# Optimization experiments

Measured on AMD Instinct MI355X. Metric: run time of the kernel, lower is better.

Reference implementation:

```python
import jax, jax.numpy as jnp
import numpy as np

N = 65536    # nodes per node type
E = 1048576  # edges per edge type
D = 512      # feature dim
B = 64       # graphs in batch


def _ln(x, g, b):
    m = x.mean(-1, keepdims=True)
    v = ((x - m) ** 2).mean(-1, keepdims=True)
    return (x - m) / jnp.sqrt(v + 1e-5) * g + b


def _seg_softmax(logits, seg, n):
    m = jax.ops.segment_max(logits, seg, num_segments=n)
    e = jnp.exp(logits - m[seg])
    s = jax.ops.segment_sum(e, seg, num_segments=n)
    return e / s[seg]


def setup_inputs():
    key = jax.random.key(0)
    k = jax.random.split(key, 16)
    sc = 1.0 / np.sqrt(D)
    d = {}
    d["x_inst"] = jax.random.normal(k[0], (N, D), jnp.float32)
    d["x_net"] = jax.random.normal(k[1], (N, D), jnp.float32)
    d["ln_g_inst"] = jnp.ones((D,), jnp.float32)
    d["ln_b_inst"] = jnp.zeros((D,), jnp.float32)
    d["ln_g_net"] = jnp.ones((D,), jnp.float32)
    d["ln_b_net"] = jnp.zeros((D,), jnp.float32)
    d["Wkqv_inst"] = jax.random.normal(k[2], (D, 3), jnp.float32) * sc
    d["bkqv_inst"] = jnp.zeros((3,), jnp.float32)
    d["Wkqv_net"] = jax.random.normal(k[3], (D, 3), jnp.float32) * sc
    d["bkqv_net"] = jnp.zeros((3,), jnp.float32)
    d["k_rel_w"] = jax.random.normal(k[4], (2,), jnp.float32)
    d["k_rel_b"] = jnp.zeros((2,), jnp.float32)
    d["v_rel_w"] = jax.random.normal(k[5], (2,), jnp.float32)
    d["v_rel_b"] = jnp.zeros((2,), jnp.float32)
    d["p_rel"] = jnp.ones((2,), jnp.float32)  # per-edge-type attention prior (heads=1)
    d["w_out_inst"] = jax.random.normal(k[6], (), jnp.float32)
    d["b_out_inst"] = jnp.zeros((), jnp.float32)
    d["w_out_net"] = jax.random.normal(k[7], (), jnp.float32)
    d["b_out_net"] = jnp.zeros((), jnp.float32)
    d["W_mlp_inst"] = jax.random.normal(k[8], (2 * D, D), jnp.float32) / np.sqrt(2 * D)
    d["b_mlp_inst"] = jnp.zeros((D,), jnp.float32)
    d["W_mlp_net"] = jax.random.normal(k[9], (2 * D, D), jnp.float32) / np.sqrt(2 * D)
    d["b_mlp_net"] = jnp.zeros((D,), jnp.float32)
    d["ei_i2n"] = jax.random.randint(k[10], (2, E), 0, N)
    d["ei_n2i"] = jax.random.randint(k[11], (2, E), 0, N)
    d["batch_inst"] = jnp.sort(jax.random.randint(k[12], (N,), 0, B))
    d["batch_net"] = jnp.sort(jax.random.randint(k[13], (N,), 0, B))
    return d


def _forward(x_inst, x_net, ln_g_inst, ln_b_inst, ln_g_net, ln_b_net,
             Wkqv_inst, bkqv_inst, Wkqv_net, bkqv_net,
             k_rel_w, k_rel_b, v_rel_w, v_rel_b, p_rel,
             w_out_inst, b_out_inst, w_out_net, b_out_net,
             W_mlp_inst, b_mlp_inst, W_mlp_net, b_mlp_net,
             ei_i2n, ei_n2i, batch_inst, batch_net):
    # LayerNorm per node over features
    xn_i = _ln(x_inst, ln_g_inst, ln_b_inst)
    xn_n = _ln(x_net, ln_g_net, ln_b_net)

    # HGTConv with out_channels=1, heads=1, head_dim=1: kqv are scalar per node
    kqv_i = xn_i @ Wkqv_inst + bkqv_inst  # [N, 3]
    kqv_n = xn_n @ Wkqv_net + bkqv_net
    k_i, q_i, v_i = kqv_i[:, 0], kqv_i[:, 1], kqv_i[:, 2]
    k_n, q_n, v_n = kqv_n[:, 0], kqv_n[:, 1], kqv_n[:, 2]

    def het_attn(k_src, v_src, q_dst, ei, rel):
        src, dst = ei[0], ei[1]
        kt = k_src * k_rel_w[rel] + k_rel_b[rel]  # per-relation K transform
        vt = v_src * v_rel_w[rel] + v_rel_b[rel]  # per-relation V transform
        # head_dim = 1 -> sqrt(D_head) = 1
        logits = q_dst[dst] * kt[src] * p_rel[rel]
        a = _seg_softmax(logits, dst, N)  # segment softmax over incoming edges
        return jax.ops.segment_sum(a * vt[src], dst, num_segments=N)  # [N]

    aggr_net = het_attn(k_i, v_i, q_n, ei_i2n, 0)   # edge type 0: inst -> net
    aggr_inst = het_attn(k_n, v_n, q_i, ei_n2i, 1)  # edge type 1: net -> inst

    # out_lin (1->1) + GELU; skip connection is skipped since 1 != D
    score_inst = jax.nn.gelu(aggr_inst * w_out_inst + b_out_inst, approximate=False)
    score_net = jax.nn.gelu(aggr_net * w_out_net + b_out_net, approximate=False)

    def pool(xn, score, batch, W, b):
        s = _seg_softmax(score, batch, B)              # softmax of scores per graph
        xw = xn * s[:, None]                           # [N, D]
        x_add = jax.ops.segment_sum(xw, batch, num_segments=B)
        x_max = jax.ops.segment_max(xw, batch, num_segments=B)
        return jnp.concatenate([x_add, x_max], axis=-1) @ W + b  # [B, D]

    out_inst = pool(xn_i, score_inst, batch_inst, W_mlp_inst, b_mlp_inst)
    out_net = pool(xn_n, score_net, batch_net, W_mlp_net, b_mlp_net)
    return jnp.concatenate([out_inst, out_net], axis=-1)  # [B, 2*D]


def reference(x_inst, x_net, ln_g_inst, ln_b_inst, ln_g_net, ln_b_net,
              Wkqv_inst, bkqv_inst, Wkqv_net, bkqv_net,
              k_rel_w, k_rel_b, v_rel_w, v_rel_b, p_rel,
              w_out_inst, b_out_inst, w_out_net, b_out_net,
              W_mlp_inst, b_mlp_inst, W_mlp_net, b_mlp_net,
              ei_i2n, ei_n2i, batch_inst, batch_net):
    return _forward(x_inst, x_net, ln_g_inst, ln_b_inst, ln_g_net, ln_b_net,
                    Wkqv_inst, bkqv_inst, Wkqv_net, bkqv_net,
                    k_rel_w, k_rel_b, v_rel_w, v_rel_b, p_rel,
                    w_out_inst, b_out_inst, w_out_net, b_out_net,
                    W_mlp_inst, b_mlp_inst, W_mlp_net, b_mlp_net,
                    ei_i2n, ei_n2i, batch_inst, batch_net)
```

## Files before the change

kernel.cpp:

```cpp
#include <hip/hip_runtime.h>
#include <math.h>
#include <float.h>

#define NN 65536
#define EE 1048576
#define DD 512
#define BB 64
#define SPLIT 8
#define CAP 4608

__device__ __forceinline__ void fadd(float* p, float v) {
    unsafeAtomicAdd(p, v);
}

__device__ __forceinline__ int lowerb(const int* __restrict__ a, int n, int v) {
    int lo = 0, hi = n;
    while (lo < hi) { int mid = (lo + hi) >> 1; if (a[mid] < v) lo = mid + 1; else hi = mid; }
    return lo;
}

__device__ __forceinline__ float dot4(float4 a, float4 b) {
    return fmaf(a.x, b.x, fmaf(a.y, b.y, fmaf(a.z, b.z, a.w * b.w)));
}

__global__ __launch_bounds__(512) void prep_kernel(
    const float* __restrict__ g_i, const float* __restrict__ b_i,
    const float* __restrict__ g_n, const float* __restrict__ b_n,
    const float* __restrict__ W_i, const float* __restrict__ bk_i,
    const float* __restrict__ W_n, const float* __restrict__ bk_n,
    float* __restrict__ gw, float* __restrict__ cAB)
{
    int t = blockIdx.x;
    const float* g  = t ? g_n : g_i;
    const float* b  = t ? b_n : b_i;
    const float* W  = t ? W_n : W_i;
    const float* bk = t ? bk_n : bk_i;
    int d = threadIdx.x;
    float gv = g[d], bv = b[d];
    float w0 = W[d * 3 + 0], w1 = W[d * 3 + 1], w2 = W[d * 3 + 2];
    float v0 = gv * w0, v1 = gv * w1, v2 = gv * w2;
    gw[((size_t)t * 3 + 0) * DD + d] = v0;
    gw[((size_t)t * 3 + 1) * DD + d] = v1;
    gw[((size_t)t * 3 + 2) * DD + d] = v2;
    __shared__ float red[8];
    float vals[6] = { v0, v1, v2, bv * w0, bv * w1, bv * w2 };
    #pragma unroll
    for (int c = 0; c < 6; ++c) {
        float v = vals[c];
        #pragma unroll
        for (int o = 32; o; o >>= 1) v += __shfl_xor(v, o);
        if ((d & 63) == 0) red[d >> 6] = v;
        __syncthreads();
        if (d == 0) {
            float sum = 0.0f;
            #pragma unroll
            for (int w = 0; w < 8; ++w) sum += red[w];
            cAB[t * 8 + c] = sum + (c >= 3 ? bk[c - 3] : 0.0f);
        }
        __syncthreads();
    }
}

__global__ __launch_bounds__(256) void ln_kqv_kernel(
    const float* __restrict__ x_i, const float* __restrict__ x_n,
    const float* __restrict__ gw, const float* __restrict__ cAB,
    const float* __restrict__ krw, const float* __restrict__ krb,
    const float* __restrict__ vrw, const float* __restrict__ vrb,
    const float* __restrict__ prel,
    float* __restrict__ mean_o, float* __restrict__ rstd_o,
    float* __restrict__ ktvt, float* __restrict__ qp)
{
    const int t  = blockIdx.x >> 14;
    const int nb = blockIdx.x & 16383;
    const float* x = t ? x_n : x_i;
    const int lane = threadIdx.x & 63;
    const int n = nb * 4 + (threadIdx.x >> 6);
    const float4* xr = (const float4*)(x + (size_t)n * DD);
    float4 xa = xr[lane];
    float4 xb = xr[lane + 64];
    const float4* g0 = (const float4*)(gw + ((size_t)t * 3 + 0) * DD);
    const float4* g1 = (const float4*)(gw + ((size_t)t * 3 + 1) * DD);
    const float4* g2 = (const float4*)(gw + ((size_t)t * 3 + 2) * DD);
    float4 w0a = g0[lane], w0b = g0[lane + 64];
    float4 w1a = g1[lane], w1b = g1[lane + 64];
    float4 w2a = g2[lane], w2b = g2[lane + 64];
    float s  = xa.x + xa.y + xa.z + xa.w + xb.x + xb.y + xb.z + xb.w;
    float ss = dot4(xa, xa)  + dot4(xb, xb);
    float p0 = dot4(xa, w0a) + dot4(xb, w0b);
    float p1 = dot4(xa, w1a) + dot4(xb, w1b);
    float p2 = dot4(xa, w2a) + dot4(xb, w2b);
    #pragma unroll
    for (int o = 32; o; o >>= 1) {
        s  += __shfl_xor(s,  o);
        ss += __shfl_xor(ss, o);
        p0 += __shfl_xor(p0, o);
        p1 += __shfl_xor(p1, o);
        p2 += __shfl_xor(p2, o);
    }
    if (lane == 0) {
        float mean = s * (1.0f / DD);
        float var  = ss * (1.0f / DD) - mean * mean;
        float rstd = rsqrtf(var + 1e-5f);
        const float* c = cAB + t * 8;
        float kv = rstd * (p0 - mean * c[0]) + c[3];
        float qv = rstd * (p1 - mean * c[1]) + c[4];
        float vv = rstd * (p2 - mean * c[2]) + c[5];
        int relk = t, relq = 1 - t;
        int gn = t * NN + n;
        mean_o[gn] = mean; rstd_o[gn] = rstd;
        ktvt[2 * gn]     = kv * krw[relk] + krb[relk];
        ktvt[2 * gn + 1] = vv * vrw[relk] + vrb[relk];
        qp[gn]           = qv * prel[relq];
    }
}

__global__ __launch_bounds__(512) void edge_scatter_kernel(
    const int* __restrict__ ei_i2n, const int* __restrict__ ei_n2i,
    const float* __restrict__ ktvt, const float* __restrict__ qp,
    int* __restrict__ cursor, float2* __restrict__ pay, unsigned char* __restrict__ fb)
{
    __shared__ int hist[256];
    __shared__ int base[256];
    int es = blockIdx.x >> 8;
    int wg = blockIdx.x & 255;
    int tid = threadIdx.x;
    if (tid < 256) hist[tid] = 0;
    __syncthreads();
    const int* ei = es ? ei_n2i : ei_i2n;
    int soff = es ? NN : 0;
    int qoff = es ? 0 : NN;
    int r    = es ? 0 : 1;
    float e_[8], ev_[8]; int br_[8];
    int ebase = wg * 4096;
    #pragma unroll
    for (int j = 0; j < 8; ++j) {
        int idx = ebase + j * 512 + tid;
        int src = ei[idx], dst = ei[EE + idx];
        float2 kv = ((const float2*)ktvt)[soff + src];
        float e = __expf(qp[qoff + dst] * kv.x);
        e_[j] = e; ev_[j] = e * kv.y;
        int bin = dst >> 8;
        int rank = atomicAdd(&hist[bin], 1);
        br_[j] = (bin << 21) | ((dst & 255) << 13) | rank;
    }
    __syncthreads();
    if (tid < 256) {
        int c = hist[tid];
        base[tid] = c ? atomicAdd(&cursor[r * 256 + tid], c) : 0;
    }
    __syncthreads();
    #pragma unroll
    for (int j = 0; j < 8; ++j) {
        int br = br_[j];
        int bin = br >> 21, f = (br >> 13) & 255, rank = br & 8191;
        int slot = base[bin] + rank;
        if (slot < CAP) {
            size_t a = (size_t)(r * 256 + bin) * CAP + slot;
            float2 p; p.x = e_[j]; p.y = ev_[j];
            pay[a] = p;
            fb[a] = (unsigned char)f;
        }
    }
}

__global__ __launch_bounds__(256) void bucket_reduce_kernel(
    const int* __restrict__ cursor, const float2* __restrict__ pay,
    const unsigned char* __restrict__ fb, float2* __restrict__ S)
{
    __shared__ float b0[256], b1[256];
    int r = blockIdx.x >> 8, c = blockIdx.x & 255;
    int tid = threadIdx.x;
    b0[tid] = 0.0f; b1[tid] = 0.0f;
    __syncthreads();
    int cnt = min(cursor[r * 256 + c], CAP);
    size_t bb = (size_t)(r * 256 + c) * CAP;
    for (int i = tid; i < cnt; i += 256) {
        float2 p = pay[bb + i];
        int f = fb[bb + i];
        atomicAdd(&b0[f], p.x);
        atomicAdd(&b1[f], p.y);
    }
    __syncthreads();
    float2 o; o.x = b0[tid]; o.y = b1[tid];
    S[r * NN + c * 256 + tid] = o;
}

__global__ __launch_bounds__(256) void score_bsum_kernel(
    const float2* __restrict__ S,
    const float* __restrict__ wout_i, const float* __restrict__ bout_i,
    const float* __restrict__ wout_n, const float* __restrict__ bout_n,
    const int* __restrict__ batch_i, const int* __restrict__ batch_n,
    float* __restrict__ esc, float* __restrict__ bsum)
{
    __shared__ float lsum[BB];
    int tid = threadIdx.x;
    if (tid < BB) lsum[tid] = 0.0f;
    __syncthreads();
    int idx = blockIdx.x * 256 + tid;
    int t = idx >> 16;
    int n = idx & (NN - 1);
    float2 sv = S[idx];
    float aggr = (sv.x > 0.0f) ? sv.y / sv.x : 0.0f;
    float w  = t ? wout_n[0] : wout_i[0];
    float b0 = t ? bout_n[0] : bout_i[0];
    float z  = fmaf(aggr, w, b0);
    float sc = 0.5f * z * (1.0f + erff(z * 0.70710678118654752440f));
    float e  = __expf(sc);
    esc[idx] = e;
    int bb = t ? batch_n[n] : batch_i[n];
    atomicAdd(&lsum[bb], e);
    __syncthreads();
    if (tid < BB && lsum[tid] != 0.0f) fadd(&bsum[t * BB + tid], lsum[tid]);
}

__global__ __launch_bounds__(512) void pool_kernel(
    const float* __restrict__ x_i, const float* __restrict__ x_n,
    const float* __restrict__ g_i, const float* __restrict__ gbi,
    const float* __restrict__ g_n, const float* __restrict__ gbn,
    const float* __restrict__ mean_, const float* __restrict__ rstd_,
    const float* __restrict__ esc, const int* __restrict__ batch_i,
    const int* __restrict__ batch_n, const float* __restrict__ bsum,
    float* __restrict__ addp, float* __restrict__ mxp)
{
    int gi = blockIdx.x;
    int t    = gi >> 9;
    int bi   = gi & 511;
    int b    = bi >> 3;
    int part = bi & (SPLIT - 1);
    const float* x     = t ? x_n : x_i;
    const float* gw    = t ? g_n : g_i;
    const float* gb    = t ? gbn : gbi;
    const int*   batch = t ? batch_n : batch_i;
    const float* mean  = mean_ + (size_t)t * NN;
    const float* rstd  = rstd_ + (size_t)t * NN;
    const float* es    = esc   + (size_t)t * NN;
    int start = lowerb(batch, NN, b);
    int end   = lowerb(batch, NN, b + 1);
    int len   = end - start;
    int chunk = (len + SPLIT - 1) / SPLIT;
    int i0 = start + part * chunk;
    int i1 = min(i0 + chunk, end);
    if (i0 > i1) i1 = i0;
    int tid = threadIdx.x;
    float gv = gw[tid], bv = gb[tid];
    float inv = 1.0f / bsum[t * BB + b];
    float acc = 0.0f, amx = -FLT_MAX;
    int i = i0;
    for (; i + 4 <= i1; i += 4) {
        float w0 = es[i]   * inv, w1 = es[i+1] * inv;
        float w2 = es[i+2] * inv, w3 = es[i+3] * inv;
        float m0 = mean[i],   m1 = mean[i+1], m2 = mean[i+2], m3 = mean[i+3];
        float r0 = rstd[i],   r1 = rstd[i+1], r2 = rstd[i+2], r3 = rstd[i+3];
        float x0 = x[(size_t)(i+0) * DD + tid];
        float x1 = x[(size_t)(i+1) * DD + tid];
        float x2 = x[(size_t)(i+2) * DD + tid];
        float x3 = x[(size_t)(i+3) * DD + tid];
        float v0 = ((x0 - m0) * r0 * gv + bv) * w0;
        float v1 = ((x1 - m1) * r1 * gv + bv) * w1;
        float v2 = ((x2 - m2) * r2 * gv + bv) * w2;
        float v3 = ((x3 - m3) * r3 * gv + bv) * w3;
        acc += v0 + v1 + v2 + v3;
        amx = fmaxf(amx, fmaxf(fmaxf(v0, v1), fmaxf(v2, v3)));
    }
    for (; i < i1; ++i) {
        float w  = es[i] * inv;
        float xv = x[(size_t)i * DD + tid];
        float v  = ((xv - mean[i]) * rstd[i] * gv + bv) * w;
        acc += v;
        amx = fmaxf(amx, v);
    }
    size_t po = ((size_t)(t * BB + b) * SPLIT + part) * DD + tid;
    addp[po] = acc;
    mxp[po]  = amx;
}

__global__ __launch_bounds__(512) void pool_reduce_kernel(
    const float* __restrict__ addp, const float* __restrict__ mxp,
    float* __restrict__ addf, float* __restrict__ mxf)
{
    int tid = threadIdx.x;
    size_t base = (size_t)blockIdx.x * SPLIT * DD + tid;
    float a = 0.0f, m = -FLT_MAX;
    #pragma unroll
    for (int p = 0; p < SPLIT; ++p) {
        a += addp[base + (size_t)p * DD];
        m = fmaxf(m, mxp[base + (size_t)p * DD]);
    }
    addf[(size_t)blockIdx.x * DD + tid] = a;
    mxf[(size_t)blockIdx.x * DD + tid]  = m;
}

__global__ __launch_bounds__(512) void mlp_kernel(
    const float* __restrict__ addf, const float* __restrict__ mxf,
    const float* __restrict__ Wm_i, const float* __restrict__ bm_i,
    const float* __restrict__ Wm_n, const float* __restrict__ bm_n,
    float* __restrict__ out)
{
    __shared__ float cat[2 * DD];
    __shared__ float psum[8][DD];
    int t = blockIdx.x >> 6;
    int b = blockIdx.x & 63;
    int tid = threadIdx.x;
    cat[tid]      = addf[(size_t)blockIdx.x * DD + tid];
    cat[DD + tid] = mxf[(size_t)blockIdx.x * DD + tid];
    __syncthreads();
    const float* W = t ? Wm_n : Wm_i;
    int w = tid >> 6, lane = tid & 63;
    float acc[8] = {0, 0, 0, 0, 0, 0, 0, 0};
    int k0 = w * 128;
    for (int k = k0; k < k0 + 128; ++k) {
        float c = cat[k];
        #pragma unroll
        for (int j = 0; j < 8; ++j)
            acc[j] = fmaf(c, W[(size_t)k * DD + lane + 64 * j], acc[j]);
    }
    #pragma unroll
    for (int j = 0; j < 8; ++j) psum[w][lane + 64 * j] = acc[j];
    __syncthreads();
    float r = (t ? bm_n : bm_i)[tid];
    #pragma unroll
    for (int wv = 0; wv < 8; ++wv) r += psum[wv][tid];
    out[(size_t)b * (2 * DD) + t * DD + tid] = r;
}

extern "C" void kernel_launch(void* const* d_in, const int* in_sizes, int n_in,
                              void* d_out, int out_size, void* d_ws, size_t ws_size,
                              hipStream_t stream)
{
    const float* x_inst = (const float*)d_in[0];
    const float* x_net  = (const float*)d_in[1];
    const float* lng_i  = (const float*)d_in[2];
    const float* lnb_i  = (const float*)d_in[3];
    const float* lng_n  = (const float*)d_in[4];
    const float* lnb_n  = (const float*)d_in[5];
    const float* Wkqv_i = (const float*)d_in[6];
    const float* bkqv_i = (const float*)d_in[7];
    const float* Wkqv_n = (const float*)d_in[8];
    const float* bkqv_n = (const float*)d_in[9];
    const float* krw    = (const float*)d_in[10];
    const float* krb    = (const float*)d_in[11];
    const float* vrw    = (const float*)d_in[12];
    const float* vrb    = (const float*)d_in[13];
    const float* prel   = (const float*)d_in[14];
    const float* wout_i = (const float*)d_in[15];
    const float* bout_i = (const float*)d_in[16];
    const float* wout_n = (const float*)d_in[17];
    const float* bout_n = (const float*)d_in[18];
    const float* Wm_i   = (const float*)d_in[19];
    const float* bm_i   = (const float*)d_in[20];
    const float* Wm_n   = (const float*)d_in[21];
    const float* bm_n   = (const float*)d_in[22];
    const int* ei_i2n   = (const int*)d_in[23];
    const int* ei_n2i   = (const int*)d_in[24];
    const int* batch_i  = (const int*)d_in[25];
    const int* batch_n  = (const int*)d_in[26];

    float* base   = (float*)d_ws;
    float* mean_  = base;
    float* rstd_  = base +  2 * (size_t)NN;
    float* ktvt   = base +  4 * (size_t)NN;
    float* qp     = base +  8 * (size_t)NN;
    float* esc    = base + 10 * (size_t)NN;
    float2* S     = (float2*)(base + 12 * (size_t)NN);
    int*   cursor = (int*)(base + 16 * (size_t)NN);
    float* bsum   = base + 16 * (size_t)NN + 512;
    float* addp   = bsum + 256;
    float* mxp    = addp + 2 * BB * SPLIT * DD;
    float* addf   = mxp  + 2 * BB * SPLIT * DD;
    float* mxf    = addf + 2 * BB * DD;
    float2* pay   = (float2*)(mxf + 2 * BB * DD);
    unsigned char* fbb = (unsigned char*)(pay + 2 * 256 * (size_t)CAP);
    float* gw     = (float*)(fbb + 2 * 256 * (size_t)CAP);
    float* cAB    = gw + 2 * 3 * DD;

    (void)hipMemsetAsync(cursor, 0, (512 + 256) * sizeof(int), stream);

    prep_kernel<<<2, 512, 0, stream>>>(lng_i, lnb_i, lng_n, lnb_n,
        Wkqv_i, bkqv_i, Wkqv_n, bkqv_n, gw, cAB);

    ln_kqv_kernel<<<2 * NN / 4, 256, 0, stream>>>(x_inst, x_net, gw, cAB,
        krw, krb, vrw, vrb, prel, mean_, rstd_, ktvt, qp);

    edge_scatter_kernel<<<512, 512, 0, stream>>>(ei_i2n, ei_n2i, ktvt, qp,
        cursor, pay, fbb);

    bucket_reduce_kernel<<<512, 256, 0, stream>>>(cursor, pay, fbb, S);

    score_bsum_kernel<<<2 * NN / 256, 256, 0, stream>>>(S,
        wout_i, bout_i, wout_n, bout_n, batch_i, batch_n, esc, bsum);

    pool_kernel<<<2 * BB * SPLIT, 512, 0, stream>>>(x_inst, x_net,
        lng_i, lnb_i, lng_n, lnb_n, mean_, rstd_, esc, batch_i, batch_n,
        bsum, addp, mxp);

    pool_reduce_kernel<<<2 * BB, 512, 0, stream>>>(addp, mxp, addf, mxf);

    mlp_kernel<<<2 * BB, 512, 0, stream>>>(addf, mxf, Wm_i, bm_i, Wm_n, bm_n,
        (float*)d_out);
}
```

Measured before the change: 485.7 us.

## Process multiple rows per wave in LN/KQV with DPP reductions and packed stats

The LayerNorm/KQV kernel now has each wave handle 8 rows, prefetching the next row while reducing the current one. Weight vectors and scalar parameters are loaded once per wave instead of once per row, and the cross-lane butterfly shuffles are replaced by DPP row/broadcast adds that leave the total in lane 63. Mean and rstd are stored as one float2 array, which pool_kernel now reads with a single load per row. The aims are to amortize setup loads and cut shuffle cost and store transactions; the trade-off is fewer blocks, so less parallelism to hide latency.

```diff
diff --git a/kernel.cpp b/kernel.cpp
--- a/kernel.cpp
+++ b/kernel.cpp
@@ -8,6 +8,7 @@
 #define BB 64
 #define SPLIT 8
 #define CAP 4608
+#define RPW 8
 
 __device__ __forceinline__ void fadd(float* p, float v) {
     unsafeAtomicAdd(p, v);
@@ -21,6 +22,23 @@
 
 __device__ __forceinline__ float dot4(float4 a, float4 b) {
     return fmaf(a.x, b.x, fmaf(a.y, b.y, fmaf(a.z, b.z, a.w * b.w)));
+}
+
+template<int CTRL>
+__device__ __forceinline__ float dppadd(float v) {
+    union { float f; int i; } u, r;
+    u.f = v;
+    r.i = __builtin_amdgcn_update_dpp(0, u.i, CTRL, 0xF, 0xF, true);
+    return v + r.f;
+}
+__device__ __forceinline__ float wave_sum63(float v) {
+    v = dppadd<0x111>(v);
+    v = dppadd<0x112>(v);
+    v = dppadd<0x114>(v);
+    v = dppadd<0x118>(v);
+    v = dppadd<0x142>(v);
+    v = dppadd<0x143>(v);
+    return v;
 }
 
 __global__ __launch_bounds__(512) void prep_kernel(
@@ -67,50 +85,60 @@
     const float* __restrict__ krw, const float* __restrict__ krb,
     const float* __restrict__ vrw, const float* __restrict__ vrb,
     const float* __restrict__ prel,
-    float* __restrict__ mean_o, float* __restrict__ rstd_o,
-    float* __restrict__ ktvt, float* __restrict__ qp)
-{
-    const int t  = blockIdx.x >> 14;
-    const int nb = blockIdx.x & 16383;
+    float2* __restrict__ mr_o, float2* __restrict__ ktvt2, float* __restrict__ qp)
+{
+    const int t  = blockIdx.x >> 11;
+    const int nb = blockIdx.x & 2047;
     const float* x = t ? x_n : x_i;
     const int lane = threadIdx.x & 63;
-    const int n = nb * 4 + (threadIdx.x >> 6);
-    const float4* xr = (const float4*)(x + (size_t)n * DD);
-    float4 xa = xr[lane];
-    float4 xb = xr[lane + 64];
+    const int w    = threadIdx.x >> 6;
+    const int row0 = nb * (4 * RPW) + w * RPW;
+
     const float4* g0 = (const float4*)(gw + ((size_t)t * 3 + 0) * DD);
     const float4* g1 = (const float4*)(gw + ((size_t)t * 3 + 1) * DD);
     const float4* g2 = (const float4*)(gw + ((size_t)t * 3 + 2) * DD);
     float4 w0a = g0[lane], w0b = g0[lane + 64];
     float4 w1a = g1[lane], w1b = g1[lane + 64];
     float4 w2a = g2[lane], w2b = g2[lane + 64];
-    float s  = xa.x + xa.y + xa.z + xa.w + xb.x + xb.y + xb.z + xb.w;
-    float ss = dot4(xa, xa)  + dot4(xb, xb);
-    float p0 = dot4(xa, w0a) + dot4(xb, w0b);
-    float p1 = dot4(xa, w1a) + dot4(xb, w1b);
-    float p2 = dot4(xa, w2a) + dot4(xb, w2b);
-    #pragma unroll
-    for (int o = 32; o; o >>= 1) {
-        s  += __shfl_xor(s,  o);
-        ss += __shfl_xor(ss, o);
-        p0 += __shfl_xor(p0, o);
-        p1 += __shfl_xor(p1, o);
-        p2 += __shfl_xor(p2, o);
-    }
-    if (lane == 0) {
-        float mean = s * (1.0f / DD);
-        float var  = ss * (1.0f / DD) - mean * mean;
-        float rstd = rsqrtf(var + 1e-5f);
-        const float* c = cAB + t * 8;
-        float kv = rstd * (p0 - mean * c[0]) + c[3];
-        float qv = rstd * (p1 - mean * c[1]) + c[4];
-        float vv = rstd * (p2 - mean * c[2]) + c[5];
-        int relk = t, relq = 1 - t;
-        int gn = t * NN + n;
-        mean_o[gn] = mean; rstd_o[gn] = rstd;
-        ktvt[2 * gn]     = kv * krw[relk] + krb[relk];
-        ktvt[2 * gn + 1] = vv * vrw[relk] + vrb[relk];
-        qp[gn]           = qv * prel[relq];
+    const float* c = cAB + t * 8;
+    float c0 = c[0], c1 = c[1], c2 = c[2], c3 = c[3], c4 = c[4], c5 = c[5];
+    const int relk = t, relq = 1 - t;
+    float ksc = krw[relk], kbi = krb[relk];
+    float vsc = vrw[relk], vbi = vrb[relk];
+    float psc = prel[relq];
+
+    const float4* xr = (const float4*)(x + (size_t)row0 * DD);
+    float4 xa = xr[lane], xb = xr[lane + 64];
+    #pragma unroll
+    for (int r = 0; r < RPW; ++r) {
+        float4 na, nb2;
+        if (r + 1 < RPW) {
+            const float4* nx = (const float4*)(x + (size_t)(row0 + r + 1) * DD);
+            na = nx[lane]; nb2 = nx[lane + 64];
+        }
+        float s  = xa.x + xa.y + xa.z + xa.w + xb.x + xb.y + xb.z + xb.w;
+        float ss = dot4(xa, xa)  + dot4(xb, xb);
+        float p0 = dot4(xa, w0a) + dot4(xb, w0b);
+        float p1 = dot4(xa, w1a) + dot4(xb, w1b);
+        float p2 = dot4(xa, w2a) + dot4(xb, w2b);
+        s  = wave_sum63(s);
+        ss = wave_sum63(ss);
+        p0 = wave_sum63(p0);
+        p1 = wave_sum63(p1);
+        p2 = wave_sum63(p2);
+        if (lane == 63) {
+            float mean = s * (1.0f / DD);
+            float var  = ss * (1.0f / DD) - mean * mean;
+            float rstd = rsqrtf(var + 1e-5f);
+            float kv = rstd * (p0 - mean * c0) + c3;
+            float qv = rstd * (p1 - mean * c1) + c4;
+            float vv = rstd * (p2 - mean * c2) + c5;
+            int gn = t * NN + row0 + r;
+            mr_o[gn]  = make_float2(mean, rstd);
+            ktvt2[gn] = make_float2(kv * ksc + kbi, vv * vsc + vbi);
+            qp[gn]    = qv * psc;
+        }
+        xa = na; xb = nb2;
     }
 }
 
@@ -217,9 +245,9 @@
     const float* __restrict__ x_i, const float* __restrict__ x_n,
     const float* __restrict__ g_i, const float* __restrict__ gbi,
     const float* __restrict__ g_n, const float* __restrict__ gbn,
-    const float* __restrict__ mean_, const float* __restrict__ rstd_,
-    const float* __restrict__ esc, const int* __restrict__ batch_i,
-    const int* __restrict__ batch_n, const float* __restrict__ bsum,
+    const float2* __restrict__ mr_, const float* __restrict__ esc,
+    const int* __restrict__ batch_i, const int* __restrict__ batch_n,
+    const float* __restrict__ bsum,
     float* __restrict__ addp, float* __restrict__ mxp)
 {
     int gi = blockIdx.x;
@@ -231,9 +259,8 @@
     const float* gw    = t ? g_n : g_i;
     const float* gb    = t ? gbn : gbi;
     const int*   batch = t ? batch_n : batch_i;
-    const float* mean  = mean_ + (size_t)t * NN;
-    const float* rstd  = rstd_ + (size_t)t * NN;
-    const float* es    = esc   + (size_t)t * NN;
+    const float2* mr   = mr_ + (size_t)t * NN;
+    const float* es    = esc + (size_t)t * NN;
     int start = lowerb(batch, NN, b);
     int end   = lowerb(batch, NN, b + 1);
     int len   = end - start;
@@ -249,23 +276,23 @@
     for (; i + 4 <= i1; i += 4) {
         float w0 = es[i]   * inv, w1 = es[i+1] * inv;
         float w2 = es[i+2] * inv, w3 = es[i+3] * inv;
-        float m0 = mean[i],   m1 = mean[i+1], m2 = mean[i+2], m3 = mean[i+3];
-        float r0 = rstd[i],   r1 = rstd[i+1], r2 = rstd[i+2], r3 = rstd[i+3];
+        float2 q0 = mr[i],   q1 = mr[i+1], q2 = mr[i+2], q3 = mr[i+3];
         float x0 = x[(size_t)(i+0) * DD + tid];
         float x1 = x[(size_t)(i+1) * DD + tid];
         float x2 = x[(size_t)(i+2) * DD + tid];
         float x3 = x[(size_t)(i+3) * DD + tid];
-        float v0 = ((x0 - m0) * r0 * gv + bv) * w0;
-        float v1 = ((x1 - m1) * r1 * gv + bv) * w1;
-        float v2 = ((x2 - m2) * r2 * gv + bv) * w2;
-        float v3 = ((x3 - m3) * r3 * gv + bv) * w3;
+        float v0 = ((x0 - q0.x) * q0.y * gv + bv) * w0;
+        float v1 = ((x1 - q1.x) * q1.y * gv + bv) * w1;
+        float v2 = ((x2 - q2.x) * q2.y * gv + bv) * w2;
+        float v3 = ((x3 - q3.x) * q3.y * gv + bv) * w3;
         acc += v0 + v1 + v2 + v3;
         amx = fmaxf(amx, fmaxf(fmaxf(v0, v1), fmaxf(v2, v3)));
     }
     for (; i < i1; ++i) {
         float w  = es[i] * inv;
+        float2 q = mr[i];
         float xv = x[(size_t)i * DD + tid];
-        float v  = ((xv - mean[i]) * rstd[i] * gv + bv) * w;
+        float v  = ((xv - q.x) * q.y * gv + bv) * w;
         acc += v;
         amx = fmaxf(amx, v);
     }
@@ -356,8 +383,7 @@
     const int* batch_n  = (const int*)d_in[26];
 
     float* base   = (float*)d_ws;
-    float* mean_  = base;
-    float* rstd_  = base +  2 * (size_t)NN;
+    float2* mr    = (float2*)base;
     float* ktvt   = base +  4 * (size_t)NN;
     float* qp     = base +  8 * (size_t)NN;
     float* esc    = base + 10 * (size_t)NN;
@@ -378,8 +404,8 @@
     prep_kernel<<<2, 512, 0, stream>>>(lng_i, lnb_i, lng_n, lnb_n,
         Wkqv_i, bkqv_i, Wkqv_n, bkqv_n, gw, cAB);
 
-    ln_kqv_kernel<<<2 * NN / 4, 256, 0, stream>>>(x_inst, x_net, gw, cAB,
-        krw, krb, vrw, vrb, prel, mean_, rstd_, ktvt, qp);
+    ln_kqv_kernel<<<2 * NN / (4 * RPW), 256, 0, stream>>>(x_inst, x_net, gw, cAB,
+        krw, krb, vrw, vrb, prel, mr, (float2*)ktvt, qp);
 
     edge_scatter_kernel<<<512, 512, 0, stream>>>(ei_i2n, ei_n2i, ktvt, qp,
         cursor, pay, fbb);
@@ -390,7 +416,7 @@
         wout_i, bout_i, wout_n, bout_n, batch_i, batch_n, esc, bsum);
 
     pool_kernel<<<2 * BB * SPLIT, 512, 0, stream>>>(x_inst, x_net,
-        lng_i, lnb_i, lng_n, lnb_n, mean_, rstd_, esc, batch_i, batch_n,
+        lng_i, lnb_i, lng_n, lnb_n, mr, esc, batch_i, batch_n,
         bsum, addp, mxp);
 
     pool_reduce_kernel<<<2 * BB, 512, 0, stream>>>(addp, mxp, addf, mxf);
```

Result: no change. 489.6 us (+0.8%).
